# Performance work log

Hardware: AMD Instinct MI355X
Metric: run time of the kernel (lower is better)

## Reference

```python
import jax, jax.numpy as jnp
import numpy as np

BETA_F = 1000.0
BETA_B = 1.0
CLAMP = 12.0
B, C, H, W = 4, 1, 1024, 1024
N_NODES = 262144  # nodes per max-tree


def soft_mask(logits):
    # forward sigmoid with beta_f gain and +-12 clamp (clamp_logits=True)
    return jax.nn.sigmoid(jnp.clip(BETA_F * logits, -CLAMP, CLAMP))


def tree_filter(sigma, levels, parent):
    """Differentiable connected filtering on one max-tree.
    Node value = level(root) + sum over root->node path of sigma_j*(level_j - level_parent_j),
    computed with pointer-doubling ancestor sums (log N gather passes).
    sigma, levels: (N,), parent: (N,) int32 with parent[0]==0 (root).
    """
    N = sigma.shape[0]
    delta = levels - levels[parent]          # per-node gray-level increment
    c = (sigma * delta).at[0].set(levels[0])  # root contributes its level
    # sentinel node N with contribution 0 and self-pointer, terminates chains
    acc = jnp.concatenate([c, jnp.zeros((1,), c.dtype)])
    ptr = jnp.concatenate([parent.at[0].set(N), jnp.full((1,), N, parent.dtype)])
    steps = int(np.ceil(np.log2(N))) + 1
    for _ in range(steps):
        acc, ptr = acc + acc[ptr], ptr[ptr]
    return acc[:N]


def setup_inputs() -> dict:
    rng = np.random.default_rng(0)
    T = B * C  # one tree per (b, c) image
    idx = np.arange(N_NODES)
    # topologically ordered random tree: parent[i] in [0, i), parent[0] = 0
    parent = np.floor(rng.random((T, N_NODES)) * idx).astype(np.int32)
    # monotone increasing gray levels: ancestor-sum of positive increments
    inc = (rng.random((T, N_NODES)) + 0.1).astype(np.float32)
    acc = np.concatenate([inc, np.zeros((T, 1), np.float32)], 1)
    ptr = np.concatenate([parent, np.full((T, 1), N_NODES, np.int64)], 1)
    ptr[:, 0] = N_NODES
    for _ in range(int(np.ceil(np.log2(N_NODES))) + 1):
        acc = acc + np.take_along_axis(acc, ptr, 1)
        ptr = np.take_along_axis(ptr, ptr, 1)
    levels = acc[:, :N_NODES]
    attr_norm = rng.random((T, N_NODES)).astype(np.float32)  # minmax01-normalized attribute
    pixel_to_node = rng.integers(0, N_NODES, (T, H * W)).astype(np.int32)
    x = rng.standard_normal((B, C, H, W)).astype(np.float32)
    return {
        "x": jnp.asarray(x),
        "attr_norm": jnp.asarray(attr_norm),
        "levels": jnp.asarray(levels),
        "thr": jnp.full((1,), 0.5, jnp.float32),  # torch init.constant_(p, 0.5)
        "parent": jnp.asarray(parent),
        "pixel_to_node": jnp.asarray(pixel_to_node),
    }


def reference(x, attr_norm, levels, thr, parent, pixel_to_node):
    # logits = attr_scaled - threshold_norm, per node, per tree
    sigma = soft_mask(attr_norm - thr.reshape(()))          # (T, N)
    v = jax.vmap(tree_filter)(sigma, levels, parent)         # (T, N) filtered node values
    y = jnp.take_along_axis(v, pixel_to_node, axis=1)        # node -> pixel gather
    return y.reshape(B, C, H, W)  # top_hat=False, num_groups=1 -> out_channels=C
```

## Files before the change

### kernel.cpp

```cpp
#include <hip/hip_runtime.h>

#define NT 4
#define NN 262144
#define NMASK (NN - 1)
#define HW 1048576
#define KPRE 8192

typedef int   vi4 __attribute__((ext_vector_type(4)));
typedef float vf4 __attribute__((ext_vector_type(4)));

#define SWIZ(b, tree, chunk)                \
    int tree  = ((b) & 7) >> 1;             \
    int chunk = (((b) >> 3) << 1) | ((b) & 1);

__global__ __launch_bounds__(1024) void k_prefix(const float* __restrict__ attr,
                                                 const float* __restrict__ levels,
                                                 const float* __restrict__ thr,
                                                 const int* __restrict__ parent,
                                                 float* __restrict__ v) {
    __shared__ float lvcs[KPRE];
    __shared__ unsigned short ps[KPRE];
    int tree = blockIdx.x;
    int tbase = tree << 18;
    float t0 = thr[0];

    for (int j = threadIdx.x; j < KPRE; j += 1024) {
        lvcs[j] = levels[tbase + j];
        ps[j] = (unsigned short)(parent[tbase + j] & (KPRE - 1));
    }
    __syncthreads();

    float creg[8];
#pragma unroll
    for (int k = 0; k < 8; ++k) {
        int j = threadIdx.x + k * 1024;
        float lv = lvcs[j];
        float lp = lvcs[ps[j]];
        float z = 1000.0f * (attr[tbase + j] - t0);
        z = fminf(fmaxf(z, -12.0f), 12.0f);
        float s = 1.0f / (1.0f + __expf(-z));
        creg[k] = (j == 0) ? lv : s * (lv - lp);
    }
    __syncthreads();
#pragma unroll
    for (int k = 0; k < 8; ++k) lvcs[threadIdx.x + k * 1024] = creg[k];
    __syncthreads();

    int   cur[8];
    float acc[8];
    int alive = 0xFF;
#pragma unroll
    for (int k = 0; k < 8; ++k) { cur[k] = threadIdx.x + k * 1024; acc[k] = 0.0f; }
    for (int it = 0; it < 64 && __any(alive); ++it) {
#pragma unroll
        for (int k = 0; k < 8; ++k) {
            if (alive & (1 << k)) {
                int c_ = cur[k];
                acc[k] += lvcs[c_];
                if (c_ == 0) alive &= ~(1 << k);
                else cur[k] = ps[c_];
            }
        }
    }
#pragma unroll
    for (int k = 0; k < 8; ++k)
        v[tbase + threadIdx.x + k * 1024] = acc[k];
}

__global__ __launch_bounds__(256) void k_build(const float* __restrict__ attr,
                                               const float* __restrict__ levels,
                                               const float* __restrict__ thr,
                                               const int* __restrict__ parent,
                                               int2* __restrict__ cmb) {
    SWIZ(blockIdx.x, tree, chunk)
    int tbase = tree << 18;
    int idx4 = KPRE / 4 + chunk * 256 + threadIdx.x;
    vi4 p4 = __builtin_nontemporal_load(&((const vi4*)(parent + tbase))[idx4]);
    vf4 a4 = __builtin_nontemporal_load(&((const vf4*)(attr + tbase))[idx4]);
    vf4 l4 = ((const vf4*)(levels + tbase))[idx4];
    float t0 = thr[0];

    int   oc[8];
#pragma unroll
    for (int e = 0; e < 4; ++e) {
        int p = p4[e] & NMASK;
        float lp = levels[tbase + p];
        float z = 1000.0f * (a4[e] - t0);
        z = fminf(fmaxf(z, -12.0f), 12.0f);
        float s = 1.0f / (1.0f + __expf(-z));
        oc[2 * e] = p;
        oc[2 * e + 1] = __float_as_int(s * (l4[e] - lp));
    }
    vi4* dst = (vi4*)(cmb + tbase);
    dst[2 * idx4]     = (vi4){oc[0], oc[1], oc[2], oc[3]};
    dst[2 * idx4 + 1] = (vi4){oc[4], oc[5], oc[6], oc[7]};
}

__global__ __launch_bounds__(256) void k_walk(const int2* __restrict__ cmb,
                                              float* __restrict__ v) {
    SWIZ(blockIdx.x, tree, chunk)
    int base = KPRE + chunk * 1024;
    const int2*  ct = cmb + (tree << 18);
    const float* vt = v + (tree << 18);

    int   cur[4];
    float acc[4];
    int alive = 0xF;
#pragma unroll
    for (int k = 0; k < 4; ++k) { cur[k] = base + threadIdx.x + k * 256; acc[k] = 0.0f; }

    for (int it = 0; it < 64 && __any(alive); ++it) {
#pragma unroll
        for (int k = 0; k < 4; ++k) {
            if (alive & (1 << k)) {
                int2 rec = ct[cur[k]];
                acc[k] += __int_as_float(rec.y);
                int nxt = rec.x;
                if (nxt < KPRE) {
                    acc[k] += vt[nxt];
                    alive &= ~(1 << k);
                } else {
                    cur[k] = nxt;
                }
            }
        }
    }
#pragma unroll
    for (int k = 0; k < 4; ++k)
        v[(tree << 18) + base + threadIdx.x + k * 256] = acc[k];
}

__global__ __launch_bounds__(256) void k_pix(const float* __restrict__ v,
                                             const int* __restrict__ p2n,
                                             float* __restrict__ y) {
    SWIZ(blockIdx.x, tree, chunk)
    int i4 = (tree << 18) + chunk * 256 + threadIdx.x;
    vi4 idx = __builtin_nontemporal_load(&((const vi4*)p2n)[i4]);
    const float* vt = v + (tree << 18);
    vf4 o;
    o.x = vt[idx.x & NMASK];
    o.y = vt[idx.y & NMASK];
    o.z = vt[idx.z & NMASK];
    o.w = vt[idx.w & NMASK];
    __builtin_nontemporal_store(o, &((vf4*)y)[i4]);
}

extern "C" void kernel_launch(void* const* d_in, const int* in_sizes, int n_in,
                              void* d_out, int out_size, void* d_ws, size_t ws_size,
                              hipStream_t stream) {
    const float* attr   = (const float*)d_in[1];
    const float* levels = (const float*)d_in[2];
    const float* thr    = (const float*)d_in[3];
    const int*   parent = (const int*)d_in[4];
    const int*   p2n    = (const int*)d_in[5];
    float*       y      = (float*)d_out;

    int2*  cmb = (int2*)d_ws;
    float* v   = (float*)((char*)d_ws + (size_t)NT * NN * 8);

    k_prefix<<<NT, 1024, 0, stream>>>(attr, levels, thr, parent, v);
    k_build <<<NT * (NN - KPRE) / 1024, 256, 0, stream>>>(attr, levels, thr, parent, cmb);
    k_walk  <<<NT * (NN - KPRE) / 1024, 256, 0, stream>>>(cmb, v);
    k_pix   <<<NT * HW / 1024, 256, 0, stream>>>(v, p2n, y);
}
```

Before: 153.0 us.

## Fuse prefix, build, walk and pixel gather into one cooperative kernel

The four separate launches become one cooperative kernel of 1024 blocks that uses grid-wide syncs between phases. One block per tree computes the shared-memory prefix while the other blocks build the combined parent/contribution records. The prefix shrinks from 8192 to 4096 nodes so a 256-thread block can hold it. This removes launch gaps and the serial four-block prefix kernel, at the cost of grid-sync overhead, longer pointer walks (they now stop at a smaller prefix), and the loss of the nontemporal hints.

After: 418.3 us. 173% more time.

```diff
diff --git a/kernel.cpp b/kernel.cpp
--- a/kernel.cpp
+++ b/kernel.cpp
@@ -1,10 +1,13 @@
 #include <hip/hip_runtime.h>
+#include <hip/hip_cooperative_groups.h>
+
+namespace cg = cooperative_groups;
 
 #define NT 4
 #define NN 262144
 #define NMASK (NN - 1)
 #define HW 1048576
-#define KPRE 8192
+#define KPRE 4096
 
 typedef int   vi4 __attribute__((ext_vector_type(4)));
 typedef float vf4 __attribute__((ext_vector_type(4)));
@@ -13,136 +16,136 @@
     int tree  = ((b) & 7) >> 1;             \
     int chunk = (((b) >> 3) << 1) | ((b) & 1);
 
-__global__ __launch_bounds__(1024) void k_prefix(const float* __restrict__ attr,
-                                                 const float* __restrict__ levels,
-                                                 const float* __restrict__ thr,
-                                                 const int* __restrict__ parent,
-                                                 float* __restrict__ v) {
+__global__ __launch_bounds__(256, 4) void k_fused(const float* __restrict__ attr,
+                                                  const float* __restrict__ levels,
+                                                  const float* __restrict__ thr,
+                                                  const int* __restrict__ parent,
+                                                  const int* __restrict__ p2n,
+                                                  float* __restrict__ y,
+                                                  int2* __restrict__ cmb,
+                                                  float* __restrict__ v) {
     __shared__ float lvcs[KPRE];
     __shared__ unsigned short ps[KPRE];
-    int tree = blockIdx.x;
+
+    cg::grid_group grid = cg::this_grid();
+    int b = blockIdx.x;
+    SWIZ(b, tree, chunk)
     int tbase = tree << 18;
+    int tid = threadIdx.x;
     float t0 = thr[0];
 
-    for (int j = threadIdx.x; j < KPRE; j += 1024) {
-        lvcs[j] = levels[tbase + j];
-        ps[j] = (unsigned short)(parent[tbase + j] & (KPRE - 1));
-    }
-    __syncthreads();
+    if (chunk < 252) {
+        int idx4 = KPRE / 4 + chunk * 256 + tid;
+        vi4 p4 = ((const vi4*)(parent + tbase))[idx4];
+        vf4 a4 = ((const vf4*)(attr + tbase))[idx4];
+        vf4 l4 = ((const vf4*)(levels + tbase))[idx4];
+        int oc[8];
+#pragma unroll
+        for (int e = 0; e < 4; ++e) {
+            int p = p4[e] & NMASK;
+            float lp = levels[tbase + p];
+            float z = 1000.0f * (a4[e] - t0);
+            z = fminf(fmaxf(z, -12.0f), 12.0f);
+            float s = 1.0f / (1.0f + __expf(-z));
+            oc[2 * e] = p;
+            oc[2 * e + 1] = __float_as_int(s * (l4[e] - lp));
+        }
+        vi4* dst = (vi4*)(cmb + tbase);
+        dst[2 * idx4]     = (vi4){oc[0], oc[1], oc[2], oc[3]};
+        dst[2 * idx4 + 1] = (vi4){oc[4], oc[5], oc[6], oc[7]};
+    } else if (chunk == 255) {
+        for (int j = tid; j < KPRE; j += 256) {
+            lvcs[j] = levels[tbase + j];
+            ps[j] = (unsigned short)(parent[tbase + j] & (KPRE - 1));
+        }
+        __syncthreads();
+        float creg[16];
+#pragma unroll
+        for (int k = 0; k < 16; ++k) {
+            int j = tid + k * 256;
+            float lv = lvcs[j];
+            float lp = lvcs[ps[j]];
+            float z = 1000.0f * (attr[tbase + j] - t0);
+            z = fminf(fmaxf(z, -12.0f), 12.0f);
+            float s = 1.0f / (1.0f + __expf(-z));
+            creg[k] = (j == 0) ? lv : s * (lv - lp);
+        }
+        __syncthreads();
+#pragma unroll
+        for (int k = 0; k < 16; ++k) lvcs[tid + k * 256] = creg[k];
+        __syncthreads();
 
-    float creg[8];
+        int   cur[16];
+        float acc[16];
+        int alive = 0xFFFF;
 #pragma unroll
-    for (int k = 0; k < 8; ++k) {
-        int j = threadIdx.x + k * 1024;
-        float lv = lvcs[j];
-        float lp = lvcs[ps[j]];
-        float z = 1000.0f * (attr[tbase + j] - t0);
-        z = fminf(fmaxf(z, -12.0f), 12.0f);
-        float s = 1.0f / (1.0f + __expf(-z));
-        creg[k] = (j == 0) ? lv : s * (lv - lp);
-    }
-    __syncthreads();
+        for (int k = 0; k < 16; ++k) { cur[k] = tid + k * 256; acc[k] = 0.0f; }
+        for (int it = 0; it < 64 && __any(alive); ++it) {
 #pragma unroll
-    for (int k = 0; k < 8; ++k) lvcs[threadIdx.x + k * 1024] = creg[k];
-    __syncthreads();
-
-    int   cur[8];
-    float acc[8];
-    int alive = 0xFF;
-#pragma unroll
-    for (int k = 0; k < 8; ++k) { cur[k] = threadIdx.x + k * 1024; acc[k] = 0.0f; }
-    for (int it = 0; it < 64 && __any(alive); ++it) {
-#pragma unroll
-        for (int k = 0; k < 8; ++k) {
-            if (alive & (1 << k)) {
-                int c_ = cur[k];
-                acc[k] += lvcs[c_];
-                if (c_ == 0) alive &= ~(1 << k);
-                else cur[k] = ps[c_];
-            }
-        }
-    }
-#pragma unroll
-    for (int k = 0; k < 8; ++k)
-        v[tbase + threadIdx.x + k * 1024] = acc[k];
-}
-
-__global__ __launch_bounds__(256) void k_build(const float* __restrict__ attr,
-                                               const float* __restrict__ levels,
-                                               const float* __restrict__ thr,
-                                               const int* __restrict__ parent,
-                                               int2* __restrict__ cmb) {
-    SWIZ(blockIdx.x, tree, chunk)
-    int tbase = tree << 18;
-    int idx4 = KPRE / 4 + chunk * 256 + threadIdx.x;
-    vi4 p4 = __builtin_nontemporal_load(&((const vi4*)(parent + tbase))[idx4]);
-    vf4 a4 = __builtin_nontemporal_load(&((const vf4*)(attr + tbase))[idx4]);
-    vf4 l4 = ((const vf4*)(levels + tbase))[idx4];
-    float t0 = thr[0];
-
-    int   oc[8];
-#pragma unroll
-    for (int e = 0; e < 4; ++e) {
-        int p = p4[e] & NMASK;
-        float lp = levels[tbase + p];
-        float z = 1000.0f * (a4[e] - t0);
-        z = fminf(fmaxf(z, -12.0f), 12.0f);
-        float s = 1.0f / (1.0f + __expf(-z));
-        oc[2 * e] = p;
-        oc[2 * e + 1] = __float_as_int(s * (l4[e] - lp));
-    }
-    vi4* dst = (vi4*)(cmb + tbase);
-    dst[2 * idx4]     = (vi4){oc[0], oc[1], oc[2], oc[3]};
-    dst[2 * idx4 + 1] = (vi4){oc[4], oc[5], oc[6], oc[7]};
-}
-
-__global__ __launch_bounds__(256) void k_walk(const int2* __restrict__ cmb,
-                                              float* __restrict__ v) {
-    SWIZ(blockIdx.x, tree, chunk)
-    int base = KPRE + chunk * 1024;
-    const int2*  ct = cmb + (tree << 18);
-    const float* vt = v + (tree << 18);
-
-    int   cur[4];
-    float acc[4];
-    int alive = 0xF;
-#pragma unroll
-    for (int k = 0; k < 4; ++k) { cur[k] = base + threadIdx.x + k * 256; acc[k] = 0.0f; }
-
-    for (int it = 0; it < 64 && __any(alive); ++it) {
-#pragma unroll
-        for (int k = 0; k < 4; ++k) {
-            if (alive & (1 << k)) {
-                int2 rec = ct[cur[k]];
-                acc[k] += __int_as_float(rec.y);
-                int nxt = rec.x;
-                if (nxt < KPRE) {
-                    acc[k] += vt[nxt];
-                    alive &= ~(1 << k);
-                } else {
-                    cur[k] = nxt;
+            for (int k = 0; k < 16; ++k) {
+                if (alive & (1 << k)) {
+                    int c_ = cur[k];
+                    acc[k] += lvcs[c_];
+                    if (c_ == 0) alive &= ~(1 << k);
+                    else cur[k] = ps[c_];
                 }
             }
         }
+#pragma unroll
+        for (int k = 0; k < 16; ++k)
+            v[tbase + tid + k * 256] = acc[k];
     }
+
+    grid.sync();
+
+    if (chunk < 252) {
+        int base = KPRE + chunk * 1024;
+        const int2*  ct = cmb + tbase;
+        const float* vt = v + tbase;
+        int   cur[4];
+        float acc[4];
+        int alive = 0xF;
 #pragma unroll
-    for (int k = 0; k < 4; ++k)
-        v[(tree << 18) + base + threadIdx.x + k * 256] = acc[k];
-}
+        for (int k = 0; k < 4; ++k) { cur[k] = base + tid + k * 256; acc[k] = 0.0f; }
+        for (int it = 0; it < 64 && __any(alive); ++it) {
+#pragma unroll
+            for (int k = 0; k < 4; ++k) {
+                if (alive & (1 << k)) {
+                    int2 rec = ct[cur[k]];
+                    acc[k] += __int_as_float(rec.y);
+                    int nxt = rec.x;
+                    if (nxt < KPRE) {
+                        acc[k] += vt[nxt];
+                        alive &= ~(1 << k);
+                    } else {
+                        cur[k] = nxt;
+                    }
+                }
+            }
+        }
+#pragma unroll
+        for (int k = 0; k < 4; ++k)
+            v[tbase + base + tid + k * 256] = acc[k];
+    }
 
-__global__ __launch_bounds__(256) void k_pix(const float* __restrict__ v,
-                                             const int* __restrict__ p2n,
-                                             float* __restrict__ y) {
-    SWIZ(blockIdx.x, tree, chunk)
-    int i4 = (tree << 18) + chunk * 256 + threadIdx.x;
-    vi4 idx = __builtin_nontemporal_load(&((const vi4*)p2n)[i4]);
-    const float* vt = v + (tree << 18);
-    vf4 o;
-    o.x = vt[idx.x & NMASK];
-    o.y = vt[idx.y & NMASK];
-    o.z = vt[idx.z & NMASK];
-    o.w = vt[idx.w & NMASK];
-    __builtin_nontemporal_store(o, &((vf4*)y)[i4]);
+    grid.sync();
+
+    {
+        const float* vt = v + tbase;
+        const vi4* p2n4 = (const vi4*)p2n;
+        vf4* y4 = (vf4*)y;
+#pragma unroll
+        for (int k = 0; k < 4; ++k) {
+            int i4 = tbase + chunk * 1024 + k * 256 + tid;
+            vi4 idx = p2n4[i4];
+            vf4 o;
+            o.x = vt[idx.x & NMASK];
+            o.y = vt[idx.y & NMASK];
+            o.z = vt[idx.z & NMASK];
+            o.w = vt[idx.w & NMASK];
+            y4[i4] = o;
+        }
+    }
 }
 
 extern "C" void kernel_launch(void* const* d_in, const int* in_sizes, int n_in,
@@ -158,8 +161,7 @@
     int2*  cmb = (int2*)d_ws;
     float* v   = (float*)((char*)d_ws + (size_t)NT * NN * 8);
 
-    k_prefix<<<NT, 1024, 0, stream>>>(attr, levels, thr, parent, v);
-    k_build <<<NT * (NN - KPRE) / 1024, 256, 0, stream>>>(attr, levels, thr, parent, cmb);
-    k_walk  <<<NT * (NN - KPRE) / 1024, 256, 0, stream>>>(cmb, v);
-    k_pix   <<<NT * HW / 1024, 256, 0, stream>>>(v, p2n, y);
+    void* args[] = {(void*)&attr, (void*)&levels, (void*)&thr, (void*)&parent,
+                    (void*)&p2n, (void*)&y, (void*)&cmb, (void*)&v};
+    hipLaunchCooperativeKernel((void*)k_fused, dim3(1024), dim3(256), args, 0, stream);
 }
```
